# Optimization experiments

Measured on AMD Instinct MI355X. Metric: run time of the kernel, lower is better.

The kernel has to match this reference:

```python
import jax, jax.numpy as jnp
import numpy as np

# ---- fixed structuring elements (buffers, not trainable) ----
N_SCALES = 4
BASE = 2.0
ZERO_SCALE = 1.0
PAD_VAL = 10000.0

_scales = ZERO_SCALE ** 2 * np.power(BASE, np.arange(N_SCALES)) ** 2  # t_k = 4^k
_widths = [4 * int(np.ceil(np.sqrt(s))) for s in _scales]             # 4,8,16,32
SES = [jnp.asarray([(1.0 / (4.0 * t)) * x ** 2 for x in range(-w, w + 1)],
                   dtype=jnp.float32)
       for t, w in zip(_scales, _widths)]  # SE lengths 9,17,33,65 (all odd)


def _pool1d(im, se, c, axis, is_max):
    """Weighted sliding max/min along `axis` (separable morphological op).
    out[p] = max_j padded[p+j] - c*se[j]  (dilation) or min_j padded[p+j] + c*se[j]."""
    n = se.shape[0]
    w = n // 2  # n is odd -> symmetric pad, matches torch pad1==pad2
    pad_val = -PAD_VAL if is_max else PAD_VAL
    cfg = [(0, 0)] * im.ndim
    cfg[axis] = (w, w)
    padded = jnp.pad(im, cfg, constant_values=pad_val)
    L = im.shape[axis]

    def take(j):
        return jax.lax.dynamic_slice_in_dim(padded, j, L, axis)

    win = jax.vmap(take)(jnp.arange(n))          # [n, B, C, H, W]
    se_b = se.reshape((n,) + (1,) * im.ndim)     # broadcast over image dims
    if is_max:
        return jnp.max(win - c * se_b, axis=0)
    return jnp.min(win + c * se_b, axis=0)


def _sep_dilation(im, se, c):
    tmp = _pool1d(im, se, c, axis=-1, is_max=True)   # horizontal
    return _pool1d(tmp, se, c, axis=-2, is_max=True)  # vertical


def _sep_erosion(im, se, c):
    tmp = _pool1d(im, se, c, axis=-1, is_max=False)
    return _pool1d(tmp, se, c, axis=-2, is_max=False)


def setup_inputs() -> dict:
    key = jax.random.key(0)
    k1, _ = jax.random.split(key)
    inputs = jax.random.normal(k1, (4, 8, 256, 256), dtype=jnp.float32)
    se_coef = jnp.float32(0.5)
    return {"inputs": inputs, "se_coef": se_coef}


def reference(inputs, se_coef):
    # closing = erosion(dilation(x)) per scale, stacked on new axis 2
    outs = [_sep_erosion(_sep_dilation(inputs, se, se_coef), se, se_coef)
            for se in SES]
    return jnp.stack(outs, axis=2)  # [B, C, n_scales, H, W]
```

## Files before the change

kernel.cpp:

```cpp
#include <hip/hip_runtime.h>


#define HH 256
#define WW 256
#define BC 32
#define NS 4
#define HW (HH * WW)
#define SLICE ((long)BC * HW)

template <int W> struct LdsStride { static constexpr int v = 2 * W + 256 + 4; };
#define LBUF_FLOATS (2 * 8 * 292)

template <int W, bool IS_MAX>
__device__ __forceinline__ void hpass_lds(const float* __restrict__ lw, float cw,
                                          float acc[8])
{
    const float PAD = IS_MAX ? -1e30f : 1e30f;
#pragma unroll
    for (int pp = 0; pp < 8; ++pp) acc[pp] = PAD;
#pragma unroll
    for (int u = 0; u < (8 + 2 * W) / 4; ++u) {
        const float4 vv = *(const float4*)(lw + 4 * u);
        const float vs[4] = {vv.x, vv.y, vv.z, vv.w};
#pragma unroll
        for (int pp = 0; pp < 8; ++pp) {
#pragma unroll
            for (int e = 0; e < 4; e += 2) {
                const int d1 = 4 * u + e - W - pp;
                const int d2 = d1 + 1;
                const bool ok1 = (d1 >= -W) && (d1 <= W);
                const bool ok2 = (d2 >= -W) && (d2 <= W);
                const float K1 = (float)(d1 * d1);
                const float K2 = (float)(d2 * d2);
                if (ok1 && ok2) {
                    const float c1 = IS_MAX ? fmaf(cw, -K1, vs[e])
                                            : fmaf(cw,  K1, vs[e]);
                    const float c2 = IS_MAX ? fmaf(cw, -K2, vs[e + 1])
                                            : fmaf(cw,  K2, vs[e + 1]);
                    acc[pp] = IS_MAX ? fmaxf(acc[pp], fmaxf(c1, c2))
                                     : fminf(acc[pp], fminf(c1, c2));
                } else if (ok1) {
                    const float c1 = IS_MAX ? fmaf(cw, -K1, vs[e])
                                            : fmaf(cw,  K1, vs[e]);
                    acc[pp] = IS_MAX ? fmaxf(acc[pp], c1) : fminf(acc[pp], c1);
                } else if (ok2) {
                    const float c2 = IS_MAX ? fmaf(cw, -K2, vs[e + 1])
                                            : fmaf(cw,  K2, vs[e + 1]);
                    acc[pp] = IS_MAX ? fmaxf(acc[pp], c2) : fminf(acc[pp], c2);
                }
            }
        }
    }
}

template <int W, bool IS_MAX, bool CLAMP>
__device__ __forceinline__ void vpass_core(const float* __restrict__ img, int x,
                                           int h0, float cw, float acc[8])
{
    const float PAD = IS_MAX ? -1e30f : 1e30f;
    constexpr int TOT = 8 + 2 * W;
#pragma unroll
    for (int pp = 0; pp < 8; ++pp) acc[pp] = PAD;
#pragma unroll
    for (int ch = 0; ch < TOT / 8; ++ch) {
        float v[8];
#pragma unroll
        for (int q = 0; q < 8; ++q) {
            const int h = h0 + ch * 8 + q - W;
            if (CLAMP) {
                const int hc = min(max(h, 0), HH - 1);
                const float tv = img[(long)hc * WW + x];
                v[q] = (h == hc) ? tv : PAD;
            } else {
                v[q] = img[(long)h * WW + x];
            }
        }
#pragma unroll
        for (int pp = 0; pp < 8; ++pp) {
#pragma unroll
            for (int q = 0; q < 8; q += 2) {
                const int d1 = ch * 8 + q - W - pp;
                const int d2 = d1 + 1;
                const bool ok1 = (d1 >= -W) && (d1 <= W);
                const bool ok2 = (d2 >= -W) && (d2 <= W);
                const float K1 = (float)(d1 * d1);
                const float K2 = (float)(d2 * d2);
                if (ok1 && ok2) {
                    const float c1 = IS_MAX ? fmaf(cw, -K1, v[q])
                                            : fmaf(cw,  K1, v[q]);
                    const float c2 = IS_MAX ? fmaf(cw, -K2, v[q + 1])
                                            : fmaf(cw,  K2, v[q + 1]);
                    acc[pp] = IS_MAX ? fmaxf(acc[pp], fmaxf(c1, c2))
                                     : fminf(acc[pp], fminf(c1, c2));
                } else if (ok1) {
                    const float c1 = IS_MAX ? fmaf(cw, -K1, v[q])
                                            : fmaf(cw,  K1, v[q]);
                    acc[pp] = IS_MAX ? fmaxf(acc[pp], c1) : fminf(acc[pp], c1);
                } else if (ok2) {
                    const float c2 = IS_MAX ? fmaf(cw, -K2, v[q + 1])
                                            : fmaf(cw,  K2, v[q + 1]);
                    acc[pp] = IS_MAX ? fmaxf(acc[pp], c2) : fminf(acc[pp], c2);
                }
            }
        }
    }
}

template <int W, bool IS_MAX, int NT>
__device__ __forceinline__ void run_tiles(const float* __restrict__ ip,
                                          float* __restrict__ op,
                                          int y0, float c, float* lbuf)
{
    constexpr int LS = LdsStride<W>::v;
    const float cw = c * (4.0f / (float)(W * W));
    const float PAD = IS_MAX ? -1e30f : 1e30f;
    const int x = threadIdx.x;
    const int r = threadIdx.x >> 5, t = threadIdx.x & 31;

#pragma unroll 1
    for (int i = 0; i < NT; ++i) {
        float* buf = lbuf + (i & 1) * 8 * LS;
        const int h0 = (y0 + i) * 8;

        float vacc[8];
        if (h0 >= W && h0 + 8 + W <= HH)
            vpass_core<W, IS_MAX, false>(ip, x, h0, cw, vacc);
        else
            vpass_core<W, IS_MAX, true >(ip, x, h0, cw, vacc);

#pragma unroll
        for (int q = 0; q < 8; ++q) buf[q * LS + W + x] = vacc[q];
        if (x < W) {
#pragma unroll
            for (int q = 0; q < 8; ++q) {
                buf[q * LS + x] = PAD;
                buf[q * LS + W + 256 + x] = PAD;
            }
        }
        __syncthreads();

        float acc[8];
        hpass_lds<W, IS_MAX>(buf + r * LS + 8 * t, cw, acc);
        float* o = op + (long)(h0 + r) * WW + 8 * t;
        *(float4*)(o)     = make_float4(acc[0], acc[1], acc[2], acc[3]);
        *(float4*)(o + 4) = make_float4(acc[4], acc[5], acc[6], acc[7]);
    }
}

template <bool IS_MAX>
__global__ __launch_bounds__(256, 8) void k_vh(const float* __restrict__ in,
                                               float* __restrict__ out,
                                               const float* __restrict__ cptr,
                                               long in_ks, long in_zs,
                                               long out_ks, long out_zs,
                                               int kfix, int bpz, int zbase)
{
    __shared__ __align__(16) float lbuf[LBUF_FLOATS];
    const int bid = blockIdx.x;
    int k, y0, z;
    if (kfix < 0) {
        const int rid  = bid & 255;
        const int slot = bid >> 8;
        int idx;
        if (rid < 128)      { k = 3; idx = rid * 8 + slot;
                              z = idx >> 5; y0 = idx & 31; }
        else if (rid < 192) { k = 2; idx = (rid - 128) * 8 + slot;
                              z = idx >> 4; y0 = (idx & 15) * 2; }
        else if (rid < 224) { k = 1; idx = (rid - 192) * 8 + slot;
                              z = idx >> 3; y0 = (idx & 7) * 4; }
        else if (rid < 240) { k = 0; idx = (rid - 224) * 8 + slot;
                              z = idx >> 2; y0 = (idx & 3) * 8; }
        else return;
    } else {
        k = kfix;
        const int zi = bid / bpz;
        const int yi = bid - zi * bpz;
        z = zbase + zi;
        y0 = yi * (32 / bpz);
    }
    const float c = cptr[0];
    const float* ip = in + (long)k * in_ks + (long)z * in_zs;
    float* op = out + (long)k * out_ks + (long)z * out_zs;
    switch (k) {
        case 0: run_tiles<4,  IS_MAX, 8>(ip, op, y0, c, lbuf); break;
        case 1: run_tiles<8,  IS_MAX, 4>(ip, op, y0, c, lbuf); break;
        case 2: run_tiles<16, IS_MAX, 2>(ip, op, y0, c, lbuf); break;
        case 3: run_tiles<32, IS_MAX, 1>(ip, op, y0, c, lbuf); break;
    }
}

extern "C" void kernel_launch(void* const* d_in, const int* in_sizes, int n_in,
                              void* d_out, int out_size, void* d_ws, size_t ws_size,
                              hipStream_t stream)
{
    const float* x = (const float*)d_in[0];
    const float* c = (const float*)d_in[1];
    float* out = (float*)d_out;
    float* ws  = (float*)d_ws;

    dim3 b(256);
    const size_t slice_b = (size_t)SLICE * sizeof(float);
    if (ws_size >= (size_t)NS * slice_b) {
        dim3 g(2048);
        k_vh<true ><<<g, b, 0, stream>>>(x,  ws,  c, 0,     HW, SLICE, HW,
                                         -1, 0, 0);
        k_vh<false><<<g, b, 0, stream>>>(ws, out, c, SLICE, HW, HW, (long)NS * HW,
                                         -1, 0, 0);
    } else if (ws_size >= slice_b) {
        for (int k = 0; k < NS; ++k) {
            const int bpz = 4 << k;
            dim3 g(bpz * BC);
            k_vh<true ><<<g, b, 0, stream>>>(x,  ws,  c, 0, HW, 0, HW,
                                             k, bpz, 0);
            k_vh<false><<<g, b, 0, stream>>>(ws, out, c, 0, HW, HW, (long)NS * HW,
                                             k, bpz, 0);
        }
    } else {
        for (int k = 0; k < NS; ++k) {
            const int bpz = 4 << k;
            dim3 g(bpz);
            for (int z = 0; z < BC; ++z) {
                k_vh<true ><<<g, b, 0, stream>>>(x,  ws,  c, 0, HW, 0, 0,
                                                 k, bpz, z);
                k_vh<false><<<g, b, 0, stream>>>(ws, out, c, 0, 0, HW, (long)NS * HW,
                                                 k, bpz, z);
            }
        }
    }
}
```

Before: 121.4 us.

## Fuse dilation and erosion launches into one cooperative kernel with grid sync

Replaces the two back-to-back kernel launches (dilation, then erosion) with a single cooperative kernel that runs the dilation tiles, performs a grid-wide barrier, then runs the erosion tiles. The goal is to remove one kernel launch and the gap between launches. In exchange it requires all 2048 blocks to be co-resident and pays for a grid-sync. Blocks with no work still have to reach the barrier. If the cooperative launch fails, it falls back to the old two-launch path.

```diff
diff --git a/kernel.cpp b/kernel.cpp
--- a/kernel.cpp
+++ b/kernel.cpp
@@ -1,5 +1,8 @@
 #include <hip/hip_runtime.h>
-
+#include <hip/hip_cooperative_groups.h>
+
+
+namespace cg = cooperative_groups;
 
 #define HH 256
 #define WW 256
@@ -147,6 +150,55 @@
     }
 }
 
+__device__ __forceinline__ bool decode_block(int bid, int& k, int& z, int& y0)
+{
+    const int rid  = bid & 255;
+    const int slot = bid >> 8;
+    int idx;
+    if (rid < 128)      { k = 3; idx = rid * 8 + slot;
+                          z = idx >> 5; y0 = idx & 31;        return true; }
+    else if (rid < 192) { k = 2; idx = (rid - 128) * 8 + slot;
+                          z = idx >> 4; y0 = (idx & 15) * 2;  return true; }
+    else if (rid < 224) { k = 1; idx = (rid - 192) * 8 + slot;
+                          z = idx >> 3; y0 = (idx & 7) * 4;   return true; }
+    else if (rid < 240) { k = 0; idx = (rid - 224) * 8 + slot;
+                          z = idx >> 2; y0 = (idx & 3) * 8;   return true; }
+    return false;
+}
+
+__global__ __launch_bounds__(256, 8) void k_closing(const float* __restrict__ x,
+                                                    float* __restrict__ ws,
+                                                    float* __restrict__ out,
+                                                    const float* __restrict__ cptr)
+{
+    __shared__ __align__(16) float lbuf[LBUF_FLOATS];
+    int k, z, y0;
+    const bool active = decode_block(blockIdx.x, k, z, y0);
+    const float c = cptr[0];
+
+    if (active) {
+        const float* ip = x + (long)z * HW;
+        float* op = ws + (long)k * SLICE + (long)z * HW;
+        switch (k) {
+            case 0: run_tiles<4,  true, 8>(ip, op, y0, c, lbuf); break;
+            case 1: run_tiles<8,  true, 4>(ip, op, y0, c, lbuf); break;
+            case 2: run_tiles<16, true, 2>(ip, op, y0, c, lbuf); break;
+            case 3: run_tiles<32, true, 1>(ip, op, y0, c, lbuf); break;
+        }
+    }
+    cg::this_grid().sync();
+    if (active) {
+        const float* ip = ws + (long)k * SLICE + (long)z * HW;
+        float* op = out + (long)k * HW + (long)z * (long)NS * HW;
+        switch (k) {
+            case 0: run_tiles<4,  false, 8>(ip, op, y0, c, lbuf); break;
+            case 1: run_tiles<8,  false, 4>(ip, op, y0, c, lbuf); break;
+            case 2: run_tiles<16, false, 2>(ip, op, y0, c, lbuf); break;
+            case 3: run_tiles<32, false, 1>(ip, op, y0, c, lbuf); break;
+        }
+    }
+}
+
 template <bool IS_MAX>
 __global__ __launch_bounds__(256, 8) void k_vh(const float* __restrict__ in,
                                                float* __restrict__ out,
@@ -159,18 +211,7 @@
     const int bid = blockIdx.x;
     int k, y0, z;
     if (kfix < 0) {
-        const int rid  = bid & 255;
-        const int slot = bid >> 8;
-        int idx;
-        if (rid < 128)      { k = 3; idx = rid * 8 + slot;
-                              z = idx >> 5; y0 = idx & 31; }
-        else if (rid < 192) { k = 2; idx = (rid - 128) * 8 + slot;
-                              z = idx >> 4; y0 = (idx & 15) * 2; }
-        else if (rid < 224) { k = 1; idx = (rid - 192) * 8 + slot;
-                              z = idx >> 3; y0 = (idx & 7) * 4; }
-        else if (rid < 240) { k = 0; idx = (rid - 224) * 8 + slot;
-                              z = idx >> 2; y0 = (idx & 3) * 8; }
-        else return;
+        if (!decode_block(bid, k, z, y0)) return;
     } else {
         k = kfix;
         const int zi = bid / bpz;
@@ -201,6 +242,11 @@
     dim3 b(256);
     const size_t slice_b = (size_t)SLICE * sizeof(float);
     if (ws_size >= (size_t)NS * slice_b) {
+        void* args[] = {(void*)&x, (void*)&ws, (void*)&out, (void*)&c};
+        hipError_t e = hipLaunchCooperativeKernel(
+            reinterpret_cast<const void*>(&k_closing),
+            dim3(2048), b, args, 0, stream);
+        if (e == hipSuccess) return;
         dim3 g(2048);
         k_vh<true ><<<g, b, 0, stream>>>(x,  ws,  c, 0,     HW, SLICE, HW,
                                          -1, 0, 0);
```

Measured after the change: 436.0 us. 259% more time.
